# Kernel tuning notes

Hardware: AMD Instinct MI355X
Metric: run time of the kernel (lower is better)

## Reference

```python
import jax, jax.numpy as jnp
import numpy as np

B, T, D_MODEL, H, W = 2, 3, 32, 256, 256
N_HEADS, N_LEVELS, N_POINTS = 4, 3, 4


def conv2d(x, w, b, padding=1, dilation=1):
    y = jax.lax.conv_general_dilated(
        x, w, window_strides=(1, 1),
        padding=[(padding, padding), (padding, padding)],
        rhs_dilation=(dilation, dilation),
        dimension_numbers=('NCHW', 'OIHW', 'NCHW'))
    return y + b[None, :, None, None]


def lrelu(x):
    return jnp.where(x >= 0, x, 0.1 * x)


def bilinear_sample(img, x, y):
    # img: (N,C,H,W); x,y: (N,H',W') pixel coords; zero padding outside (grid_sample zeros)
    N, C, Hh, Ww = img.shape
    x0 = jnp.floor(x); y0 = jnp.floor(y)
    lx = x - x0; ly = y - y0
    imf = img.reshape(N, C, Hh * Ww)
    out = jnp.zeros((N, C) + x.shape[1:], img.dtype)
    for dy, dx, wgt in ((0, 0, (1 - lx) * (1 - ly)), (0, 1, lx * (1 - ly)),
                        (1, 0, (1 - lx) * ly), (1, 1, lx * ly)):
        xi = x0 + dx; yi = y0 + dy
        valid = (xi >= 0) & (xi < Ww) & (yi >= 0) & (yi < Hh)
        idx = (jnp.clip(yi, 0, Hh - 1) * Ww + jnp.clip(xi, 0, Ww - 1)).astype(jnp.int32)
        g = jnp.take_along_axis(imf, idx.reshape(N, 1, -1), axis=2).reshape((N, C) + x.shape[1:])
        out = out + g * (wgt * valid)[:, None]
    return out


def flow_warp(x, flow):
    # torch flow_warp with align_corners=True == sampling at pixel coords grid+flow
    N, C, Hh, Ww = x.shape
    gy, gx = jnp.meshgrid(jnp.arange(Hh, dtype=x.dtype), jnp.arange(Ww, dtype=x.dtype), indexing='ij')
    return bilinear_sample(x, gx[None] + flow[:, 0], gy[None] + flow[:, 1])


def ms_deform_attn(value, sampling_locations, attention_weights, h, w):
    # value: (N, L*h*w, Hh, d); loc: (N, Lq, Hh, L, P, 2) in [0,1]; weights: (N, Lq, Hh, L, P)
    # Matches MSDA CUDA kernel: sample at loc*(W,H)-0.5, bilinear, zero pad outside.
    N, _, Hh, d = value.shape
    Lq = sampling_locations.shape[1]
    L, P = sampling_locations.shape[3], sampling_locations.shape[4]
    out = jnp.zeros((N, Lq, Hh, d), value.dtype)
    for l in range(L):
        v = value[:, l * h * w:(l + 1) * h * w].transpose(0, 2, 1, 3)  # (N,Hh,hw,d)
        loc = sampling_locations[:, :, :, l]  # (N,Lq,Hh,P,2)
        x = loc[..., 0] * w - 0.5
        y = loc[..., 1] * h - 0.5
        x0 = jnp.floor(x); y0 = jnp.floor(y)
        lx = x - x0; ly = y - y0
        samp = jnp.zeros((N, Lq, Hh, P, d), value.dtype)
        for dy, dx, wgt in ((0, 0, (1 - lx) * (1 - ly)), (0, 1, lx * (1 - ly)),
                            (1, 0, (1 - lx) * ly), (1, 1, lx * ly)):
            xi = x0 + dx; yi = y0 + dy
            valid = (xi >= 0) & (xi < w) & (yi >= 0) & (yi < h)
            idx = (jnp.clip(yi, 0, h - 1) * w + jnp.clip(xi, 0, w - 1)).astype(jnp.int32)
            idx = idx.transpose(0, 2, 1, 3).reshape(N, Hh, Lq * P)
            g = jnp.take_along_axis(v, idx[..., None], axis=2)  # (N,Hh,Lq*P,d)
            g = g.reshape(N, Hh, Lq, P, d).transpose(0, 2, 1, 3, 4)
            samp = samp + g * (wgt * valid)[..., None]
        out = out + (samp * attention_weights[:, :, :, l][..., None]).sum(axis=3)
    return out.reshape(N, Lq, Hh * d)


def setup_inputs() -> dict:
    key = jax.random.key(0)
    ks = jax.random.split(key, 24)
    def rn(k, shape, s=1.0):
        return jax.random.normal(k, shape, dtype=jnp.float32) * s
    c = D_MODEL
    nofp = N_HEADS * N_LEVELS * N_POINTS
    return {
        'frame': rn(ks[0], (B, T, c, H, W)),
        'srcframe': rn(ks[1], (B, T, c, H, W)),
        'flow_forward': rn(ks[2], (B, T - 1, 2, H, W), 2.0),
        'flow_backward': rn(ks[3], (B, T - 1, 2, H, W), 2.0),
        'W_qk': rn(ks[4], (3 * c, 3 * c + 4, 3, 3), 0.05), 'b_qk': rn(ks[5], (3 * c,), 0.05),
        'W_v': rn(ks[6], (3 * c, 3 * c, 3, 3), 0.05), 'b_v': rn(ks[7], (3 * c,), 0.05),
        'W_vp': rn(ks[8], (c, c, 3, 3), 0.05), 'b_vp': rn(ks[9], (c,), 0.05),
        'W_off': rn(ks[10], (nofp * 2, 3 * c, 3, 3), 0.01), 'b_off': rn(ks[11], (nofp * 2,), 0.5),
        'W_aw': rn(ks[12], (nofp, 3 * c, 3, 3), 0.05), 'b_aw': rn(ks[13], (nofp,), 0.05),
        'W_out': rn(ks[14], (c, c, 3, 3), 0.05), 'b_out': rn(ks[15], (c,), 0.05),
        'W_ffd': rn(ks[16], (c, c, 3, 3), 0.05), 'b_ffd': rn(ks[17], (c,), 0.05),
        'W_ff1': rn(ks[18], (c, 2 * c, 3, 3), 0.05), 'b_ff1': rn(ks[19], (c,), 0.05),
        'W_ff2': rn(ks[20], (c, c, 3, 3), 0.05), 'b_ff2': rn(ks[21], (c,), 0.05),
        'W_fu': rn(ks[22], (c, c, 1, 1), 0.05), 'b_fu': rn(ks[23], (c,), 0.05),
    }


def reference(frame, srcframe, flow_forward, flow_backward,
              W_qk, b_qk, W_v, b_v, W_vp, b_vp, W_off, b_off, W_aw, b_aw,
              W_out, b_out, W_ffd, b_ffd, W_ff1, b_ff1, W_ff2, b_ff2, W_fu, b_fu):
    b, t, c, h, w = frame.shape
    Hh, L, P = N_HEADS, N_LEVELS, N_POINTS
    d = c // Hh
    # flow-warped neighbor frames + flows -> query embedding
    warp01 = flow_warp(frame[:, 0], flow_backward[:, 0])
    warp21 = flow_warp(frame[:, 2], flow_forward[:, 1])
    qk_in = jnp.concatenate([warp01, frame[:, 1], warp21,
                             flow_forward[:, 1], flow_backward[:, 0]], axis=1)
    qureys = lrelu(conv2d(qk_in, W_qk, b_qk))                       # (b, 3c, h, w)
    value = conv2d(frame.reshape(b, t * c, h, w), W_v, b_v)         # (b, 3c, h, w)
    # --- MSDeformAttn_Fusion ---
    val = conv2d(value.reshape(b * t, c, h, w), W_vp, b_vp).reshape(b, t, c, h, w)
    off = conv2d(qureys, W_off, b_off)                               # (b, Hh*L*P*2, h, w)
    aw = conv2d(qureys, W_aw, b_aw)                                  # (b, Hh*L*P, h, w)
    value_flat = val.reshape(b, t, c, h * w).transpose(0, 1, 3, 2).reshape(b, t * h * w, Hh, d)
    off = off.reshape(b, -1, h * w).transpose(0, 2, 1).reshape(b, h * w, Hh, L, P, 2)
    aw = aw.reshape(b, -1, h * w).transpose(0, 2, 1).reshape(b, h * w, Hh, L * P)
    aw = jax.nn.softmax(aw, axis=-1).reshape(b, h * w, Hh, L, P)
    # reference points: pixel centers normalized (masks all zero -> valid_ratios == 1)
    gy, gx = jnp.meshgrid((jnp.arange(h, dtype=off.dtype) + 0.5) / h,
                          (jnp.arange(w, dtype=off.dtype) + 0.5) / w, indexing='ij')
    ref = jnp.stack([gx.reshape(-1), gy.reshape(-1)], -1)            # (hw, 2) (x, y)
    normalizer = jnp.array([w, h], dtype=off.dtype)                  # same for all levels
    loc = ref[None, :, None, None, None, :] + off / normalizer
    attn_out = ms_deform_attn(value_flat, loc, aw, h, w)             # (b, hw, c)
    out = attn_out.reshape(b, h, w, c).transpose(0, 3, 1, 2)
    out = conv2d(out, W_out, b_out)                                  # output_proj
    # --- post-attention ---
    out = conv2d(out, W_ffd, b_ffd) + frame[:, 1]
    tseq = jnp.concatenate([out, srcframe[:, 1]], axis=1)            # (b, 2c, h, w)
    ff = conv2d(lrelu(conv2d(tseq, W_ff1, b_ff1, padding=2, dilation=2)), W_ff2, b_ff2)
    out = out + ff
    out = lrelu(conv2d(out, W_fu, b_fu, padding=0))                  # fusion 1x1
    return out
```

## Files before the change

### kernel.cpp

```cpp
#include <hip/hip_runtime.h>
#include <hip/hip_bf16.h>

typedef __hip_bfloat16 bf16;
typedef unsigned short us;
typedef unsigned int u32;
typedef __attribute__((ext_vector_type(8))) short short8;
typedef __attribute__((ext_vector_type(8))) unsigned short ushortx8;
typedef __attribute__((ext_vector_type(2))) float f32x2;
typedef __attribute__((ext_vector_type(4))) float f32x4;
typedef __attribute__((ext_vector_type(16))) float f32x16;

#define HW 65536
#define IMW 256
#define IMH 256

static __device__ __forceinline__ float u2f(us u) {
  return __uint_as_float(((unsigned)u) << 16);
}
static __device__ __forceinline__ us f2bu(float x) {
  bf16 h = __float2bfloat16(x);
  return *reinterpret_cast<us*>(&h);
}
static __device__ __forceinline__ unsigned pk2(float a, float b) {
  return (unsigned)f2bu(a) | ((unsigned)f2bu(b) << 16);
}

static __device__ __forceinline__ void gload_lds16(const void* g, void* l) {
  __builtin_amdgcn_global_load_lds(
      (const __attribute__((address_space(1))) u32*)g,
      (__attribute__((address_space(3))) u32*)l, 16, 0, 0);
}

struct PrepArgs {
  const float* src[9];
  us* dst[9];
  int OC[9], CIN[9], KPAD[9], LAY[9], KCH[9];
};

__global__ __launch_bounds__(256) void prep_weights(PrepArgs a) {
  int j = blockIdx.y;
  int n = blockIdx.x * 256 + threadIdx.x;
  int OC = a.OC[j], CIN = a.CIN[j], KPAD = a.KPAD[j];
  int tot = 9 * OC * KPAD;
  if (n >= tot) return;
  int oc, k;
  if (a.LAY[j] == 0) {
    int G = OC >> 4, NKC = KPAD >> 5;
    int e = n & 7;
    int m = (n >> 3) & 15;
    int q = (n >> 7) & 3;
    int rest = n >> 9;
    int kc = rest % NKC;
    int tg = rest / NKC;
    int g = tg % G;
    int t = tg / G;
    oc = g * 16 + m;
    k = kc * 32 + q * 8 + e;
    float v = (k < CIN) ? a.src[j][(size_t)(oc * CIN + k) * 9 + t] : 0.f;
    a.dst[j][n] = f2bu(v);
  } else {
    int OCT = OC >> 5;
    int KCH = a.KCH[j];
    int KHH = KCH >> 4;
    int e = n & 7;
    int l = (n >> 3) & 63;
    int rest = n >> 9;
    int jt = rest % OCT;
    int u = rest / OCT;
    int khi = u % KHH;
    int sg = u / KHH;
    int kc = sg / 9;
    oc = jt * 32 + (l & 31);
    k = kc * KCH + khi * 16 + (l >> 5) * 8 + e;
    int t = sg - kc * 9;
    float v = (k < CIN) ? a.src[j][(size_t)(oc * CIN + k) * 9 + t] : 0.f;
    a.dst[j][n] = f2bu(v);
  }
}

__global__ __launch_bounds__(256) void frame_to_nhwc(const float* __restrict__ frame,
                                                     unsigned* __restrict__ fn) {
  int tid = threadIdx.x;
  int half = tid & 1;
  int pix = blockIdx.x * 128 + (tid >> 1);
  int b = blockIdx.y;
  const float* s = frame + ((size_t)b * 96 + (size_t)half * 48) * HW + pix;
  unsigned u[24];
#pragma unroll
  for (int j = 0; j < 24; ++j)
    u[j] = pk2(s[(size_t)(2 * j) * HW], s[(size_t)(2 * j + 1) * HW]);
  unsigned* d = fn + ((size_t)b * HW + pix) * 48 + half * 24;
#pragma unroll
  for (int j = 0; j < 6; ++j) {
    uint4 w;
    w.x = u[4 * j]; w.y = u[4 * j + 1]; w.z = u[4 * j + 2]; w.w = u[4 * j + 3];
    *(uint4*)&d[4 * j] = w;
  }
}

static __device__ void warp_nhwc(const us* __restrict__ fn, size_t bbase, int coff,
                                 float x, float y, unsigned* uo) {
  float x0f = floorf(x), y0f = floorf(y);
  float lx = x - x0f, ly = y - y0f;
  int x0 = (int)x0f, y0 = (int)y0f;
  float wt[4] = {(1.f - lx) * (1.f - ly), lx * (1.f - ly), (1.f - lx) * ly, lx * ly};
  float acc[32] = {};
#pragma unroll
  for (int k = 0; k < 4; ++k) {
    int xi = x0 + (k & 1), yi = y0 + (k >> 1);
    if ((unsigned)xi < IMW && (unsigned)yi < IMH) {
      const ushortx8* s =
          (const ushortx8*)(fn + (bbase + (size_t)yi * IMW + xi) * 96 + coff);
      float w = wt[k];
#pragma unroll
      for (int cj = 0; cj < 4; ++cj) {
        ushortx8 vv = s[cj];
#pragma unroll
        for (int e = 0; e < 8; ++e)
          acc[cj * 8 + e] = fmaf(w, u2f(vv[e]), acc[cj * 8 + e]);
      }
    }
  }
#pragma unroll
  for (int j = 0; j < 16; ++j) uo[j] = pk2(acc[2 * j], acc[2 * j + 1]);
}

__global__ __launch_bounds__(256) void build_qkin(
    const us* __restrict__ fn, const float* __restrict__ flowf,
    const float* __restrict__ flowb, unsigned* __restrict__ qk) {
  int tid = threadIdx.x;
  int half = tid & 1;
  int pix = blockIdx.x * 128 + (tid >> 1);
  int b = blockIdx.y;
  int px = pix & 255, py = pix >> 8;
  unsigned* qb = qk + ((size_t)b * HW + pix) * 50;

  if (half == 0) {
    float fbx = flowb[((size_t)(b * 2 + 0) * 2 + 0) * HW + pix];
    float fby = flowb[((size_t)(b * 2 + 0) * 2 + 1) * HW + pix];
    unsigned u[32];
    {
      const unsigned* s = (const unsigned*)(fn + ((size_t)b * HW + pix) * 96);
#pragma unroll
      for (int j = 0; j < 16; ++j) u[16 + j] = s[16 + j];
    }
    warp_nhwc(fn, (size_t)b * HW, 0, (float)px + fbx, (float)py + fby, &u[0]);
#pragma unroll
    for (int j = 0; j < 16; ++j) {
      uint2 t;
      t.x = u[2 * j];
      t.y = u[2 * j + 1];
      *(uint2*)(qb + 2 * j) = t;
    }
  } else {
    float fbx = flowb[((size_t)(b * 2 + 0) * 2 + 0) * HW + pix];
    float fby = flowb[((size_t)(b * 2 + 0) * 2 + 1) * HW + pix];
    float ffx = flowf[((size_t)(b * 2 + 1) * 2 + 0) * HW + pix];
    float ffy = flowf[((size_t)(b * 2 + 1) * 2 + 1) * HW + pix];
    unsigned u[18];
    warp_nhwc(fn, (size_t)b * HW, 64, (float)px + ffx, (float)py + ffy, &u[0]);
    u[16] = pk2(ffx, ffy);
    u[17] = pk2(fbx, fby);
#pragma unroll
    for (int j = 0; j < 9; ++j) {
      uint2 t;
      t.x = u[2 * j];
      t.y = u[2 * j + 1];
      *(uint2*)(qb + 32 + 2 * j) = t;
    }
  }
}

template <int CIN, int CST, int KPAD, int KCH, int OCT, bool LRELU>
__global__ __launch_bounds__(256) void conv3x3_m32(
    const us* __restrict__ in, const us* __restrict__ W2,
    const float* __restrict__ bias, us* __restrict__ out, int out_cst,
    int out_coff) {
  constexpr int COLS = 34, ROWS = 10, HALO = COLS * ROWS;
  constexpr int CIPAD = KCH + 8;
  constexpr int CHc = KCH / 8;
  constexpr int KHH = KCH / 16;
  constexpr int NCH = KPAD / KCH;
  constexpr int NSTG = NCH * 9;
  constexpr int CHB = KHH * OCT;
  __shared__ alignas(16) short lds[HALO * CIPAD];
  __shared__ alignas(16) short wlds[2][CHB * 512];

  const int z = blockIdx.z;
  const int px0 = blockIdx.x * 32, py0 = blockIdx.y * 8;
  const int lane = threadIdx.x & 63;
  const int wv = threadIdx.x >> 6;
  const int n = lane & 31;
  const int sr = n >> 4;
  const int colp = n & 15;
  const int kq = lane >> 5;

  f32x16 acc[2][OCT];
#pragma unroll
  for (int f = 0; f < 2; ++f)
#pragma unroll
    for (int j = 0; j < OCT; ++j) acc[f][j] = 0.f;

  const int rb = 2 * wv + sr;
  const int base0 = ((rb + 1) * COLS + colp + 1) * CIPAD + kq * 8;
  const int base1 = base0 + 16 * CIPAD;

  int buf = 0, sg = 0;
#pragma unroll 1
  for (int kc = 0; kc < NCH; ++kc) {
    for (int c = threadIdx.x; c < HALO * CHc; c += 256) {
      int p = c / CHc, cb = c - p * CHc;
      int row = p / COLS, col = p - row * COLS;
      int gy = py0 + row - 1, gx = px0 + col - 1;
      bool ok = ((unsigned)gy < IMH) && ((unsigned)gx < IMW);
      int cil = cb * 8;
      int cig = kc * KCH + cil;
      const us* gp = in + ((size_t)z * HW + (size_t)gy * IMW + gx) * CST + cig;
      if (CIN == KPAD) {
        short8 v = (short8)0;
        if (ok) v = *(const short8*)gp;
        *(short8*)&lds[p * CIPAD + cil] = v;
      } else {
        uint2 h0; h0.x = 0; h0.y = 0;
        uint2 h1; h1.x = 0; h1.y = 0;
        if (ok && cig + 4 <= CIN) h0 = *(const uint2*)gp;
        if (ok && cig + 8 <= CIN) h1 = *(const uint2*)(gp + 4);
        *(uint2*)&lds[p * CIPAD + cil] = h0;
        *(uint2*)&lds[p * CIPAD + cil + 4] = h1;
      }
    }
    if (kc == 0) {
#pragma unroll
      for (int r = 0; r < (CHB + 3) / 4; ++r) {
        int blk = r * 4 + wv;
        if (blk < CHB)
          gload_lds16(W2 + (size_t)(blk * 64 + lane) * 8, &wlds[0][blk * 512]);
      }
    }
    __syncthreads();

#pragma unroll 1
    for (int t = 0; t < 9; ++t, ++sg) {
      if (sg + 1 < NSTG) {
        const us* wn = W2 + (size_t)(sg + 1) * (CHB * 512);
#pragma unroll
        for (int r = 0; r < (CHB + 3) / 4; ++r) {
          int blk = r * 4 + wv;
          if (blk < CHB)
            gload_lds16(wn + (size_t)(blk * 64 + lane) * 8,
                        &wlds[buf ^ 1][blk * 512]);
        }
      }
      const int dy = t / 3 - 1, dx = t - (t / 3) * 3 - 1;
      const int toff = (dy * COLS + dx) * CIPAD;
#pragma unroll
      for (int khr = 0; khr < KHH; ++khr) {
        short8 bf0 = *(const short8*)&lds[base0 + toff + khr * 16];
        short8 bf1 = *(const short8*)&lds[base1 + toff + khr * 16];
#pragma unroll
        for (int j = 0; j < OCT; ++j) {
          short8 af =
              *(const short8*)&wlds[buf][(khr * OCT + j) * 512 + lane * 8];
          acc[0][j] = __builtin_amdgcn_mfma_f32_32x32x16_bf16(af, bf0,
                                                              acc[0][j], 0, 0, 0);
          acc[1][j] = __builtin_amdgcn_mfma_f32_32x32x16_bf16(af, bf1,
                                                              acc[1][j], 0, 0, 0);
        }
      }
      __syncthreads();
      buf ^= 1;
    }
  }

  {
    int row = py0 + rb;
#pragma unroll
    for (int f = 0; f < 2; ++f) {
      int pxc = px0 + 16 * f + colp;
      us* ob =
          out + ((size_t)z * HW + (size_t)row * IMW + pxc) * out_cst + out_coff;
#pragma unroll
      for (int j = 0; j < OCT; ++j) {
#pragma unroll
        for (int hi = 0; hi < 4; ++hi) {
          int oc0 = j * 32 + hi * 8 + kq * 4;
          f32x4 bb = *(const f32x4*)&bias[oc0];
          float v0 = acc[f][j][4 * hi + 0] + bb[0];
          float v1 = acc[f][j][4 * hi + 1] + bb[1];
          float v2 = acc[f][j][4 * hi + 2] + bb[2];
          float v3 = acc[f][j][4 * hi + 3] + bb[3];
          if (LRELU) {
            v0 = v0 >= 0.f ? v0 : 0.1f * v0;
            v1 = v1 >= 0.f ? v1 : 0.1f * v1;
            v2 = v2 >= 0.f ? v2 : 0.1f * v2;
            v3 = v3 >= 0.f ? v3 : 0.1f * v3;
          }
          uint2 w;
          w.x = pk2(v0, v1);
          w.y = pk2(v2, v3);
          *(uint2*)&ob[oc0] = w;
        }
      }
    }
  }
}

template <int CIN, int CST, int KPAD, int DIL, int G, int ZDIV, int CSUB,
          int RES, int OUTMODE, bool LRELU>
__global__ __launch_bounds__(256) void conv3x3_mfma(
    const us* __restrict__ in, const us* __restrict__ W2,
    const float* __restrict__ bias, void* __restrict__ out, int out_cst,
    int out_coff, float* __restrict__ outB, const float* __restrict__ res,
    int res_cst, int res_coff) {
  constexpr int OC = G * 16;
  constexpr int COLS = 16 + 2 * DIL;
  constexpr int ROWS = 8 + 2 * DIL;
  constexpr int HALO = ROWS * COLS;
  constexpr int CIPAD = KPAD + 8;
  constexpr int CH = KPAD / 8;
  constexpr int NKC = KPAD / 32;
  constexpr int GW0 = (G + 1) / 2;
  constexpr int NU = 9 * NKC;
  __shared__ alignas(16) short lds[HALO * CIPAD];

  const int z = blockIdx.z;
  const int bin = z / ZDIV;
  const int coff = (z % ZDIV) * CSUB;
  const int px0 = blockIdx.x * 16, py0 = blockIdx.y * 8;
  const int lane = threadIdx.x & 63;
  const int wv = threadIdx.x >> 6;
  const int m = lane & 15, q = lane >> 4;
  const int gh = wv & 1, rh = wv >> 1;
  const int goff = gh * GW0;

  f32x4 acc[GW0][4];
#pragma unroll
  for (int g = 0; g < GW0; ++g)
#pragma unroll
    for (int r = 0; r < 4; ++r) acc[g][r] = 0.f;

  for (int c = threadIdx.x; c < HALO * CH; c += 256) {
    int p = c / CH, cb = c - p * CH;
    int row = p / COLS, col = p - row * COLS;
    int gy = py0 + row - DIL, gx = px0 + col - DIL;
    bool ok = ((unsigned)gy < IMH) && ((unsigned)gx < IMW);
    int ci0 = cb * 8;
    const us* gp = in + ((size_t)bin * HW + (size_t)gy * IMW + gx) * CST + coff + ci0;
    if (CIN == KPAD) {
      short8 v = (short8)0;
      if (ok) v = *(const short8*)gp;
      *(short8*)&lds[p * CIPAD + ci0] = v;
    } else {
      uint2 h0; h0.x = 0; h0.y = 0;
      uint2 h1; h1.x = 0; h1.y = 0;
      if (ok && ci0 + 4 <= CIN) h0 = *(const uint2*)gp;
      if (ok && ci0 + 8 <= CIN) h1 = *(const uint2*)(gp + 4);
      *(uint2*)&lds[p * CIPAD + ci0] = h0;
      *(uint2*)&lds[p * CIPAD + ci0 + 4] = h1;
    }
  }
  __syncthreads();

  const us* wl = W2 + (size_t)lane * 8;
  short8 af[2][GW0];
#pragma unroll
  for (int g = 0; g < GW0; ++g)
    if (goff + g < G)
      af[0][g] = *(const short8*)(wl + (size_t)((goff + g) * NKC) * 512);

#pragma unroll
  for (int u = 0; u < NU; ++u) {
    const int t = u / NKC, kc = u - t * NKC;
    if (u + 1 < NU) {
      const int t1 = (u + 1) / NKC, kc1 = (u + 1) - t1 * NKC;
#pragma unroll
      for (int g = 0; g < GW0; ++g)
        if (goff + g < G)
          af[(u + 1) & 1][g] =
              *(const short8*)(wl + (size_t)((t1 * G + goff + g) * NKC + kc1) * 512);
    }
    const int dy = t / 3 - 1, dx = t - (t / 3) * 3 - 1;
    short8 bfr[4];
#pragma unroll
    for (int r = 0; r < 4; ++r) {
      int rr = rh * 4 + r + DIL + dy * DIL;
      int cc = m + DIL + dx * DIL;
      bfr[r] = *(const short8*)&lds[(rr * COLS + cc) * CIPAD + kc * 32 + q * 8];
    }
#pragma unroll
    for (int g = 0; g < GW0; ++g)
      if (goff + g < G)
#pragma unroll
        for (int r = 0; r < 4; ++r)
          acc[g][r] = __builtin_amdgcn_mfma_f32_16x16x32_bf16(af[u & 1][g], bfr[r],
                                                              acc[g][r], 0, 0, 0);
  }

#pragma unroll
  for (int g = 0; g < GW0; ++g) {
    if (goff + g < G) {
      int oc0 = (goff + g) * 16 + q * 4;
      f32x4 bb = *(const f32x4*)&bias[oc0];
#pragma unroll
      for (int r = 0; r < 4; ++r) {
        int py = py0 + rh * 4 + r;
        int px = px0 + m;
        size_t pix = (size_t)py * IMW + px;
        f32x4 v;
#pragma unroll
        for (int e = 0; e < 4; ++e) {
          float x = acc[g][r][e] + bb[e];
          if (LRELU) x = x >= 0.f ? x : 0.1f * x;
          v[e] = x;
        }
        if (RES == 1) {
          f32x4 rv = *(const f32x4*)&res[((size_t)z * HW + pix) * res_cst + oc0];
#pragma unroll
          for (int e = 0; e < 4; ++e) v[e] += rv[e];
        }
        if (RES == 2) {
#pragma unroll
          for (int e = 0; e < 4; ++e)
            v[e] += res[((size_t)z * res_cst + res_coff + oc0 + e) * HW + pix];
        }
        if (OUTMODE == 0 || OUTMODE == 3) {
          uint2 w;
          w.x = pk2(v[0], v[1]);
          w.y = pk2(v[2], v[3]);
          *(uint2*)&((us*)out)[((size_t)z * HW + pix) * out_cst + out_coff + oc0] = w;
        }
        if (OUTMODE == 2)
          *(f32x4*)&((float*)out)[((size_t)z * HW + pix) * out_cst + oc0] = v;
        if (OUTMODE == 3)
          *(f32x4*)&outB[((size_t)z * HW + pix) * 32 + oc0] = v;
      }
    }
  }
}

__global__ __launch_bounds__(256) void deform_attn(
    const us* __restrict__ valp, const us* __restrict__ off,
    const float* __restrict__ aw, us* __restrict__ outp) {
  int tid = threadIdx.x;
  int half = tid & 1;
  int hh = (tid >> 1) & 3;
  int pix = blockIdx.x * 32 + (tid >> 3);
  int b = blockIdx.y;
  int px = pix & (IMW - 1), py = pix >> 8;

  us os[12];
  {
    const uint2* ob = (const uint2*)(off + ((size_t)b * HW + pix) * 96 +
                                     hh * 24 + half * 12);
    uint2 a0 = ob[0], a1 = ob[1], a2 = ob[2];
    *(uint2*)&os[0] = a0;
    *(uint2*)&os[4] = a1;
    *(uint2*)&os[8] = a2;
  }
  float wv[6];
  {
    const f32x2* ab = (const f32x2*)(aw + ((size_t)b * HW + pix) * 48 +
                                     hh * 12 + half * 6);
    f32x2 a0 = ab[0], a1 = ab[1], a2 = ab[2];
    wv[0] = a0.x; wv[1] = a0.y; wv[2] = a1.x;
    wv[3] = a1.y; wv[4] = a2.x; wv[5] = a2.y;
  }

  float m6 = wv[0];
#pragma unroll
  for (int i = 1; i < 6; ++i) m6 = fmaxf(m6, wv[i]);
  float mx = fmaxf(m6, __shfl_xor(m6, 1));
  float s6 = 0.f;
#pragma unroll
  for (int i = 0; i < 6; ++i) {
    wv[i] = __expf(wv[i] - mx);
    s6 += wv[i];
  }
  float inv = 1.f / (s6 + __shfl_xor(s6, 1));

  f32x2 acc2[4];
#pragma unroll
  for (int j = 0; j < 4; ++j) acc2[j] = 0.f;

#pragma unroll
  for (int i = 0; i < 6; ++i) {
    int pp = half * 6 + i;
    int l = pp >> 2;
    const us* vbase = valp + ((size_t)(b * 3 + l) * HW) * 32 + hh * 8;
    float x = (float)px + u2f(os[2 * i]);
    float y = (float)py + u2f(os[2 * i + 1]);
    float x0f = floorf(x), y0f = floorf(y);
    float lx = x - x0f, ly = y - y0f;
    int x0 = (int)x0f, y0 = (int)y0f;
    bool vx0 = (unsigned)x0 < IMW, vx1 = (unsigned)(x0 + 1) < IMW;
    bool vy0 = (unsigned)y0 < IMH, vy1 = (unsigned)(y0 + 1) < IMH;
    float a = wv[i] * inv;
    float ax0 = (1.f - lx) * a, ax1 = lx * a;
    float w00 = ax0 * (1.f - ly), w01 = ax1 * (1.f - ly);
    float w10 = ax0 * ly, w11 = ax1 * ly;
    const us* p00 = vbase + (size_t)((long)(y0 * IMW + x0)) * 32;
#pragma unroll
    for (int c = 0; c < 4; ++c) {
      bool ok = (c & 1 ? vx1 : vx0) && (c & 2 ? vy1 : vy0);
      float w = (c == 0) ? w00 : (c == 1) ? w01 : (c == 2) ? w10 : w11;
      const us* p = p00 + (c & 1) * 32 + (c >> 1) * (IMW * 32);
      if (ok) {
        uint4 uu = *(const uint4*)p;
        unsigned uarr[4] = {uu.x, uu.y, uu.z, uu.w};
#pragma unroll
        for (int j = 0; j < 4; ++j) {
          f32x2 v;
          v.x = __uint_as_float(uarr[j] << 16);
          v.y = __uint_as_float(uarr[j] & 0xffff0000u);
          acc2[j] += v * w;
        }
      }
    }
  }

  float accf[8];
#pragma unroll
  for (int j = 0; j < 4; ++j) {
    accf[2 * j] = acc2[j].x + __shfl_xor(acc2[j].x, 1);
    accf[2 * j + 1] = acc2[j].y + __shfl_xor(acc2[j].y, 1);
  }
  if (half == 0) {
    ushortx8 sv;
#pragma unroll
    for (int dd = 0; dd < 8; ++dd) sv[dd] = f2bu(accf[dd]);
    *(ushortx8*)(outp + ((size_t)b * HW + pix) * 32 + hh * 8) = sv;
  }
}

__global__ __launch_bounds__(256) void copy_src(const float* __restrict__ src,
                                                unsigned* __restrict__ out1b) {
  int pix = blockIdx.x * 256 + threadIdx.x;
  int b = blockIdx.y;
  const float* s = src + ((size_t)(b * 3 + 1) * 32) * HW + pix;
  unsigned u[16];
#pragma unroll
  for (int j = 0; j < 16; ++j)
    u[j] = pk2(s[(size_t)(2 * j) * HW], s[(size_t)(2 * j + 1) * HW]);
  unsigned* d = out1b + ((size_t)b * HW + pix) * 32 + 16;
#pragma unroll
  for (int j = 0; j < 4; ++j) {
    uint4 w;
    w.x = u[4 * j]; w.y = u[4 * j + 1]; w.z = u[4 * j + 2]; w.w = u[4 * j + 3];
    *(uint4*)&d[4 * j] = w;
  }
}

__global__ __launch_bounds__(256) void conv1x1_fu(
    const float* __restrict__ in, const float* __restrict__ wgt,
    const float* __restrict__ bias, float* __restrict__ out) {
  int pix = blockIdx.x * 256 + threadIdx.x;
  int b = blockIdx.y;
  int oc0 = blockIdx.z * 16;
  float vin[32];
  {
    const f32x4* s = (const f32x4*)(in + ((size_t)b * HW + pix) * 32);
#pragma unroll
    for (int j = 0; j < 8; ++j) {
      f32x4 v = s[j];
#pragma unroll
      for (int e = 0; e < 4; ++e) vin[4 * j + e] = v[e];
    }
  }
#pragma unroll 1
  for (int oc = oc0; oc < oc0 + 16; ++oc) {
    float a = bias[oc];
#pragma unroll
    for (int ci = 0; ci < 32; ++ci) a = fmaf(wgt[oc * 32 + ci], vin[ci], a);
    a = a >= 0.f ? a : 0.1f * a;
    out[((size_t)b * 32 + oc) * HW + pix] = a;
  }
}

extern "C" void kernel_launch(void* const* d_in, const int* in_sizes, int n_in,
                              void* d_out, int out_size, void* d_ws, size_t ws_size,
                              hipStream_t stream) {
  (void)in_sizes; (void)n_in; (void)out_size;
  if (ws_size < 25614592ull * 4) return;

  const float* frame = (const float*)d_in[0];
  const float* srcframe = (const float*)d_in[1];
  const float* flowf = (const float*)d_in[2];
  const float* flowb = (const float*)d_in[3];

  float* ws = (float*)d_ws;
  us* wsu = (us*)d_ws;

  static const int w2off[9] = {0,      110592, 193536, 202752, 285696,
                               327168, 336384, 345600, 364032};
  us* fnhwc = (us*)(ws + 186624);
  unsigned* qk_u = (unsigned*)(ws + 6478080);
  us* qk = (us*)qk_u;
  us* Q = (us*)(ws + 13031680);
  us* V = (us*)(ws + 6478080);
  us* Vp = (us*)(ws + 19323136);
  us* offb = (us*)(ws + 186624);
  float* awb = (float*)(ws + 6478080);
  us* attn = (us*)(ws + 13031680);
  us* convout = (us*)(ws + 13031680 + 2097152);
  us* out1b = (us*)(ws + 6478080);
  unsigned* out1b_u = (unsigned*)out1b;
  float* out1f = (float*)(ws + 19323136);
  us* ff1out = (us*)(ws + 186624);
  float* out2 = (float*)(ws + 13031680);

  {
    PrepArgs pa;
    static const int srcidx[9] = {4, 6, 8, 10, 12, 14, 16, 18, 20};
    static const int OCs[9] = {96, 96, 32, 96, 48, 32, 32, 32, 32};
    static const int CINs[9] = {100, 96, 32, 96, 96, 32, 32, 64, 32};
    static const int KPADs[9] = {128, 96, 32, 96, 96, 32, 32, 64, 32};
    static const int LAYs[9] = {1, 1, 0, 1, 0, 0, 0, 0, 0};
    static const int KCHs[9] = {32, 32, 32, 32, 32, 32, 32, 32, 32};
    for (int i = 0; i < 9; ++i) {
      pa.src[i] = (const float*)d_in[srcidx[i]];
      pa.dst[i] = wsu + w2off[i];
      pa.OC[i] = OCs[i];
      pa.CIN[i] = CINs[i];
      pa.KPAD[i] = KPADs[i];
      pa.LAY[i] = LAYs[i];
      pa.KCH[i] = KCHs[i];
    }
    prep_weights<<<dim3(432, 9), 256, 0, stream>>>(pa);
  }

  frame_to_nhwc<<<dim3(512, 2), 256, 0, stream>>>(frame, (unsigned*)fnhwc);

  build_qkin<<<dim3(512, 2), 256, 0, stream>>>(fnhwc, flowf, flowb, qk_u);

  dim3 cg2(16, 32, 2);
  dim3 cg32(8, 32, 2);

  conv3x3_m32<100, 100, 128, 32, 3, true><<<cg32, 256, 0, stream>>>(
      qk, wsu + w2off[0], (const float*)d_in[5], Q, 96, 0);

  conv3x3_m32<96, 96, 96, 32, 3, false><<<cg32, 256, 0, stream>>>(
      fnhwc, wsu + w2off[1], (const float*)d_in[7], V, 96, 0);

  conv3x3_mfma<32, 96, 32, 1, 2, 3, 32, 0, 0, false><<<dim3(16, 32, 6), 256, 0, stream>>>(
      V, wsu + w2off[2], (const float*)d_in[9], Vp, 32, 0, nullptr, nullptr, 0, 0);

  conv3x3_m32<96, 96, 96, 32, 3, false><<<cg32, 256, 0, stream>>>(
      Q, wsu + w2off[3], (const float*)d_in[11], offb, 96, 0);

  conv3x3_mfma<96, 96, 96, 1, 3, 1, 0, 0, 2, false><<<cg2, 256, 0, stream>>>(
      Q, wsu + w2off[4], (const float*)d_in[13], awb, 48, 0, nullptr, nullptr, 0, 0);

  deform_attn<<<dim3(2048, 2), 256, 0, stream>>>(Vp, offb, awb, attn);

  conv3x3_mfma<32, 32, 32, 1, 2, 1, 0, 0, 0, false><<<cg2, 256, 0, stream>>>(
      attn, wsu + w2off[5], (const float*)d_in[15], convout, 32, 0, nullptr, nullptr, 0, 0);

  conv3x3_mfma<32, 32, 32, 1, 2, 1, 0, 2, 3, false><<<cg2, 256, 0, stream>>>(
      convout, wsu + w2off[6], (const float*)d_in[17], out1b, 64, 0, out1f, frame, 96, 32);

  copy_src<<<dim3(256, 2), 256, 0, stream>>>(srcframe, out1b_u);

  conv3x3_mfma<64, 64, 64, 2, 2, 1, 0, 0, 0, true><<<cg2, 256, 0, stream>>>(
      out1b, wsu + w2off[7], (const float*)d_in[19], ff1out, 32, 0, nullptr, nullptr, 0, 0);

  conv3x3_mfma<32, 32, 32, 1, 2, 1, 0, 1, 2, false><<<cg2, 256, 0, stream>>>(
      ff1out, wsu + w2off[8], (const float*)d_in[21], out2, 32, 0, nullptr, out1f, 32, 0);

  conv1x1_fu<<<dim3(256, 2, 2), 256, 0, stream>>>(out2, (const float*)d_in[22],
                                                  (const float*)d_in[23], (float*)d_out);
}
```

Measured before the change: 465.3 us.

## Triple-buffer conv weight stages with fine-grained vmcnt waits instead of full syncthreads

Weight tiles for the 3x3 MFMA conv are now prefetched two stages ahead into a three-slot LDS ring instead of one stage ahead into a double buffer. The per-stage __syncthreads is replaced by explicit s_waitcnt vmcnt with a count that leaves the newest prefetch outstanding, followed by a raw s_barrier. The aim is to hide global-to-LDS weight load latency behind MFMA work. In exchange it uses more LDS, which may reduce occupancy, and it depends on hand-counted outstanding memory operations, which is fragile if the compiler emits other vector loads.

```diff
diff --git a/kernel.cpp b/kernel.cpp
--- a/kernel.cpp
+++ b/kernel.cpp
@@ -183,8 +183,11 @@
   constexpr int NCH = KPAD / KCH;
   constexpr int NSTG = NCH * 9;
   constexpr int CHB = KHH * OCT;
+  constexpr int KQ0 = CHB / 4;
+  constexpr int KQ1 = KQ0 + 1;
+  constexpr int WTHR = CHB % 4;
   __shared__ alignas(16) short lds[HALO * CIPAD];
-  __shared__ alignas(16) short wlds[2][CHB * 512];
+  __shared__ alignas(16) short wlds[3][CHB * 512];
 
   const int z = blockIdx.z;
   const int px0 = blockIdx.x * 32, py0 = blockIdx.y * 8;
@@ -205,7 +208,7 @@
   const int base0 = ((rb + 1) * COLS + colp + 1) * CIPAD + kq * 8;
   const int base1 = base0 + 16 * CIPAD;
 
-  int buf = 0, sg = 0;
+  int cur = 0, sg = 0;
 #pragma unroll 1
   for (int kc = 0; kc < NCH; ++kc) {
     for (int c = threadIdx.x; c < HALO * CHc; c += 256) {
@@ -231,44 +234,65 @@
     }
     if (kc == 0) {
 #pragma unroll
-      for (int r = 0; r < (CHB + 3) / 4; ++r) {
-        int blk = r * 4 + wv;
-        if (blk < CHB)
-          gload_lds16(W2 + (size_t)(blk * 64 + lane) * 8, &wlds[0][blk * 512]);
+      for (int s0 = 0; s0 < 2; ++s0) {
+        if (s0 < NSTG) {
+          const us* w0 = W2 + (size_t)s0 * (CHB * 512);
+#pragma unroll
+          for (int r = 0; r < (CHB + 3) / 4; ++r) {
+            int blk = r * 4 + wv;
+            if (blk < CHB)
+              gload_lds16(w0 + (size_t)(blk * 64 + lane) * 8,
+                          &wlds[s0][blk * 512]);
+          }
+        }
       }
     }
     __syncthreads();
 
 #pragma unroll 1
     for (int t = 0; t < 9; ++t, ++sg) {
-      if (sg + 1 < NSTG) {
-        const us* wn = W2 + (size_t)(sg + 1) * (CHB * 512);
+      int nxt2 = cur + 2;
+      if (nxt2 >= 3) nxt2 -= 3;
+      const bool havenext = (sg + 2 < NSTG);
+      if (havenext) {
+        const us* wn = W2 + (size_t)(sg + 2) * (CHB * 512);
 #pragma unroll
         for (int r = 0; r < (CHB + 3) / 4; ++r) {
           int blk = r * 4 + wv;
           if (blk < CHB)
             gload_lds16(wn + (size_t)(blk * 64 + lane) * 8,
-                        &wlds[buf ^ 1][blk * 512]);
-        }
-      }
-      const int dy = t / 3 - 1, dx = t - (t / 3) * 3 - 1;
+                        &wlds[nxt2][blk * 512]);
+        }
+      }
+      const int tt = sg - kc * 9;
+      const int dy = tt / 3 - 1, dx = tt - (tt / 3) * 3 - 1;
       const int toff = (dy * COLS + dx) * CIPAD;
+      const short* wb = &wlds[cur][0];
 #pragma unroll
       for (int khr = 0; khr < KHH; ++khr) {
         short8 bf0 = *(const short8*)&lds[base0 + toff + khr * 16];
         short8 bf1 = *(const short8*)&lds[base1 + toff + khr * 16];
 #pragma unroll
         for (int j = 0; j < OCT; ++j) {
-          short8 af =
-              *(const short8*)&wlds[buf][(khr * OCT + j) * 512 + lane * 8];
+          short8 af = *(const short8*)&wb[(khr * OCT + j) * 512 + lane * 8];
           acc[0][j] = __builtin_amdgcn_mfma_f32_32x32x16_bf16(af, bf0,
                                                               acc[0][j], 0, 0, 0);
           acc[1][j] = __builtin_amdgcn_mfma_f32_32x32x16_bf16(af, bf1,
                                                               acc[1][j], 0, 0, 0);
         }
       }
-      __syncthreads();
-      buf ^= 1;
+      if (havenext) {
+        if (WTHR != 0 && wv < WTHR)
+          asm volatile("s_waitcnt vmcnt(%0)" ::"i"(KQ1) : "memory");
+        else
+          asm volatile("s_waitcnt vmcnt(%0)" ::"i"(KQ0) : "memory");
+      } else {
+        asm volatile("s_waitcnt vmcnt(0)" ::: "memory");
+      }
+      asm volatile("s_waitcnt lgkmcnt(0)" ::: "memory");
+      __builtin_amdgcn_s_barrier();
+      __builtin_amdgcn_sched_barrier(0);
+      cur = (cur == 2) ? 0 : cur + 1;
     }
   }
 
```

Measured after the change: 469.3 us. About the same (+0.8%).
